# Kernel optimization log

Hardware: AMD Instinct MI355X
Metric: run time of the kernel (lower is better)

## Reference

```python
import jax, jax.numpy as jnp
import numpy as np
import math

B, S, DIN, DOUT, H, L, R, E = 8, 512, 256, 256, 8, 4, 8, 65536
N = B * S  # graph nodes = all tokens
DEPTH = DOUT // H


def setup_inputs() -> dict:
    key = jax.random.key(0)
    ks = jax.random.split(key, 16)
    s_in = 1.0 / math.sqrt(DIN)
    s_out = 1.0 / math.sqrt(DOUT)
    return {
        "x": jax.random.normal(ks[0], (B, S, DIN), jnp.float32),
        # graph structure (constant ints)
        "edge_src": jax.random.randint(ks[1], (E,), 0, N),
        "edge_dst": jax.random.randint(ks[2], (E,), 0, N),
        "edge_type": jax.random.randint(ks[3], (E,), 0, R),
        # linear: input_size -> output_size
        "Wl": jax.random.normal(ks[4], (DOUT, DIN), jnp.float32) * s_in,
        "bl": jnp.zeros((DOUT,), jnp.float32),
        # relational GAT params per layer / relation
        "Wgat": jax.random.normal(ks[5], (L, R, DOUT, DOUT), jnp.float32) * s_out,
        "a_src": jax.random.normal(ks[6], (L, R, DOUT), jnp.float32) * s_out,
        "a_dst": jax.random.normal(ks[7], (L, R, DOUT), jnp.float32) * s_out,
        # linear1: output_size -> input_size
        "W1": jax.random.normal(ks[8], (DIN, DOUT), jnp.float32) * s_out,
        "b1": jnp.zeros((DIN,), jnp.float32),
        # Wq, Wk: input_size -> output_size
        "Wq": jax.random.normal(ks[9], (DOUT, DIN), jnp.float32) * s_in,
        "bq": jnp.zeros((DOUT,), jnp.float32),
        "Wk": jax.random.normal(ks[10], (DOUT, DIN), jnp.float32) * s_in,
        "bk": jnp.zeros((DOUT,), jnp.float32),
    }


def _segment_softmax(e, dst, n):
    m = jax.ops.segment_max(e, dst, num_segments=n)
    ex = jnp.exp(e - m[dst])
    denom = jax.ops.segment_sum(ex, dst, num_segments=n)
    return ex / (denom[dst] + 1e-16)


def _rgat(h, Wgat, a_src, a_dst, edge_src, edge_dst, edge_type):
    # h: [N, DOUT]
    for l in range(L):
        # per-relation transform of all nodes: [R, N, D]
        hr = jnp.einsum('nd,rde->rne', h, Wgat[l])
        msg = hr[edge_type, edge_src]  # [E, D] gather by (relation, src)
        logits = (jnp.sum(a_src[l][edge_type] * msg, axis=-1)
                  + jnp.sum(a_dst[l][edge_type] * h[edge_dst], axis=-1))
        alpha = _segment_softmax(jax.nn.leaky_relu(logits, 0.2), edge_dst, N)
        agg = jax.ops.segment_sum(alpha[:, None] * msg, edge_dst, num_segments=N)
        h = jax.nn.elu(agg)
    return h


def reference(x, edge_src, edge_dst, edge_type, Wl, bl, Wgat, a_src, a_dst,
              W1, b1, Wq, bq, Wk, bk):
    h = x @ Wl.T + bl                       # [B, S, DOUT]
    h = h.reshape(N, DOUT)
    h = _rgat(h, Wgat, a_src, a_dst, edge_src, edge_dst, edge_type)
    h = h.reshape(B, S, DOUT)
    h = h @ W1.T + b1                       # [B, S, DIN]
    q = (h @ Wq.T + bq).reshape(B, S, H, DEPTH).transpose(0, 2, 1, 3)
    k = (h @ Wk.T + bk).reshape(B, S, H, DEPTH).transpose(0, 2, 1, 3)
    attn = jnp.einsum('bhqd,bhkd->bhqk', q, k) / math.sqrt(DEPTH)
    return attn
```

## Files before the change

kernel.cpp:

```cpp
#include <hip/hip_runtime.h>
#include <math.h>

#define NN 4096
#define D 256
#define RR 8
#define LL 4
#define EE 65536
#define BB 8
#define SS 512
#define HH 8

typedef short bf16x8 __attribute__((ext_vector_type(8)));
typedef float f32x4 __attribute__((ext_vector_type(4)));

__device__ __forceinline__ unsigned short f2bf(float f) {
  unsigned u = __float_as_uint(f);
  unsigned r = (u + 0x7fffu + ((u >> 16) & 1u)) >> 16;
  return (unsigned short)r;
}
__device__ __forceinline__ float bf2f(unsigned short s) {
  return __uint_as_float(((unsigned)s) << 16);
}

__device__ __forceinline__ void gload16(unsigned short* dst, const unsigned short* src) {
  __builtin_amdgcn_global_load_lds(
      (const __attribute__((address_space(1))) void*)src,
      (__attribute__((address_space(3))) void*)dst, 16, 0, 0);
}

template<int BM, int BN, bool F32OUT, bool SPLITOUT>
__global__ __launch_bounds__(256) void gemm_split(
    const unsigned short* __restrict__ Ah, const unsigned short* __restrict__ Al,
    const unsigned short* __restrict__ Bh, const unsigned short* __restrict__ Bl,
    const float* __restrict__ bias,
    float* __restrict__ C, unsigned short* __restrict__ Ch, unsigned short* __restrict__ Cl,
    int M, int N, int K)
{
  constexpr int MF = BM / 32;
  constexpr int NF = BN / 32;
  constexpr int ABUF = BM * 32;
  constexpr int BBUF = BN * 32;
  constexpr int BUFSZ = 2 * ABUF + 2 * BBUF;
  __shared__ unsigned short lds[2 * BUFSZ];

  const int t = threadIdx.x;
  const int lane = t & 63;
  const int w = t >> 6;
  const int wm = w >> 1, wn = w & 1;
  const int rb = blockIdx.y * BM;
  const int cb = blockIdx.x * BN;

  f32x4 acc[MF][NF];
#pragma unroll
  for (int m = 0; m < MF; ++m)
#pragma unroll
    for (int n = 0; n < NF; ++n)
      acc[m][n] = (f32x4){0.f, 0.f, 0.f, 0.f};

  const int srow = t >> 2;
  const int lslot = (t & 3) ^ ((srow >> 1) & 3);
  const unsigned short* gAh = Ah + (size_t)(rb + srow) * K + lslot * 8;
  const unsigned short* gAl = Al + (size_t)(rb + srow) * K + lslot * 8;
  const unsigned short* gBh = Bh + (size_t)(cb + srow) * K + lslot * 8;
  const unsigned short* gBl = Bl + (size_t)(cb + srow) * K + lslot * 8;

  auto stage = [&](int buf, int k0) {
    unsigned short* p = lds + buf * BUFSZ;
#pragma unroll
    for (int i = 0; i < BM / 64; ++i) {
      gload16(p + i * 2048 + t * 8,        gAh + (size_t)i * 64 * K + k0);
      gload16(p + ABUF + i * 2048 + t * 8, gAl + (size_t)i * 64 * K + k0);
    }
#pragma unroll
    for (int i = 0; i < BN / 64; ++i) {
      gload16(p + 2 * ABUF + i * 2048 + t * 8,        gBh + (size_t)i * 64 * K + k0);
      gload16(p + 2 * ABUF + BBUF + i * 2048 + t * 8, gBl + (size_t)i * 64 * K + k0);
    }
  };

  stage(0, 0);
  int cur = 0;
  for (int k0 = 0; k0 < K; k0 += 32) {
    __syncthreads();
    if (k0 + 32 < K) stage(cur ^ 1, k0 + 32);
    const unsigned short* p = lds + cur * BUFSZ;

    bf16x8 ah[MF], al[MF];
#pragma unroll
    for (int m = 0; m < MF; ++m) {
      int row = wm * (BM / 2) + m * 16 + (lane & 15);
      int off = row * 32 + (((lane >> 4) ^ ((row >> 1) & 3)) << 3);
      ah[m] = *(const bf16x8*)(p + off);
      al[m] = *(const bf16x8*)(p + ABUF + off);
    }
#pragma unroll
    for (int n = 0; n < NF; ++n) {
      int brow = wn * (BN / 2) + n * 16 + (lane & 15);
      int boff = brow * 32 + (((lane >> 4) ^ ((brow >> 1) & 3)) << 3);
      bf16x8 bh = *(const bf16x8*)(p + 2 * ABUF + boff);
      bf16x8 bl = *(const bf16x8*)(p + 2 * ABUF + BBUF + boff);
#pragma unroll
      for (int m = 0; m < MF; ++m) {
        acc[m][n] = __builtin_amdgcn_mfma_f32_16x16x32_bf16(ah[m], bh, acc[m][n], 0, 0, 0);
        acc[m][n] = __builtin_amdgcn_mfma_f32_16x16x32_bf16(al[m], bh, acc[m][n], 0, 0, 0);
        acc[m][n] = __builtin_amdgcn_mfma_f32_16x16x32_bf16(ah[m], bl, acc[m][n], 0, 0, 0);
      }
    }
    cur ^= 1;
  }

#pragma unroll
  for (int m = 0; m < MF; ++m) {
#pragma unroll
    for (int n = 0; n < NF; ++n) {
      int row0 = rb + wm * (BM / 2) + m * 16 + (lane >> 4) * 4;
      int col = cb + wn * (BN / 2) + n * 16 + (lane & 15);
      float bv = bias ? bias[col] : 0.f;
#pragma unroll
      for (int j = 0; j < 4; ++j) {
        float v = acc[m][n][j] + bv;
        size_t idx = (size_t)(row0 + j) * N + col;
        if (F32OUT) C[idx] = v;
        if (SPLITOUT) {
          unsigned short hb = f2bf(v);
          Ch[idx] = hb;
          Cl[idx] = f2bf(v - bf2f(hb));
        }
      }
    }
  }
}

__global__ __launch_bounds__(256) void cvt2_k(const float* __restrict__ x,
    unsigned short* __restrict__ xh, unsigned short* __restrict__ xl,
    const float* __restrict__ Wl,
    unsigned short* __restrict__ wlh, unsigned short* __restrict__ wll)
{
  const float* src; unsigned short* hi; unsigned short* lo; int i;
  if (blockIdx.x < 1024) { src = x;  hi = xh;  lo = xl;  i = blockIdx.x * 256 + threadIdx.x; }
  else                   { src = Wl; hi = wlh; lo = wll; i = (blockIdx.x - 1024) * 256 + threadIdx.x; }
  float4 v = ((const float4*)src)[i];
  ushort4 h, l;
  h.x = f2bf(v.x); l.x = f2bf(v.x - bf2f(h.x));
  h.y = f2bf(v.y); l.y = f2bf(v.y - bf2f(h.y));
  h.z = f2bf(v.z); l.z = f2bf(v.z - bf2f(h.z));
  h.w = f2bf(v.w); l.w = f2bf(v.w - bf2f(h.w));
  ((ushort4*)hi)[i] = h;
  ((ushort4*)lo)[i] = l;
}

__global__ __launch_bounds__(256) void transp_split_k(const float* __restrict__ W,
    unsigned short* __restrict__ th, unsigned short* __restrict__ tl)
{
  __shared__ float s[32][33];
  int g = blockIdx.z, bi = blockIdx.y, bj = blockIdx.x;
  int t = threadIdx.x;
  int r = t >> 3, c = (t & 7) * 4;
  float4 v = *(const float4*)(W + ((size_t)g * D + bi * 32 + r) * D + bj * 32 + c);
  s[r][c + 0] = v.x; s[r][c + 1] = v.y; s[r][c + 2] = v.z; s[r][c + 3] = v.w;
  __syncthreads();
  size_t ob = ((size_t)g * D + bj * 32 + r) * D + bi * 32 + c;
  ushort4 h, l;
  float o0 = s[c + 0][r], o1 = s[c + 1][r], o2 = s[c + 2][r], o3 = s[c + 3][r];
  h.x = f2bf(o0); l.x = f2bf(o0 - bf2f(h.x));
  h.y = f2bf(o1); l.y = f2bf(o1 - bf2f(h.y));
  h.z = f2bf(o2); l.z = f2bf(o2 - bf2f(h.z));
  h.w = f2bf(o3); l.w = f2bf(o3 - bf2f(h.w));
  *(ushort4*)(th + ob) = h;
  *(ushort4*)(tl + ob) = l;
}

__global__ void count_k(const int* __restrict__ ed, int* __restrict__ cnt) {
  int e = blockIdx.x * 256 + threadIdx.x;
  if (e < EE) atomicAdd(&cnt[ed[e]], 1);
}

__global__ __launch_bounds__(1024) void scan_k(const int* __restrict__ cnt,
    int* __restrict__ off, int* __restrict__ cur) {
  __shared__ int part[1024];
  int t = threadIdx.x;
  int base = t * 4;
  int c0 = cnt[base], c1 = cnt[base+1], c2 = cnt[base+2], c3 = cnt[base+3];
  int s = c0 + c1 + c2 + c3;
  part[t] = s;
  __syncthreads();
  for (int o = 1; o < 1024; o <<= 1) {
    int v = 0;
    if (t >= o) v = part[t - o];
    __syncthreads();
    part[t] += v;
    __syncthreads();
  }
  int excl = part[t] - s;
  off[base] = excl; off[base+1] = excl + c0; off[base+2] = excl + c0 + c1;
  off[base+3] = excl + c0 + c1 + c2;
  cur[base] = excl; cur[base+1] = excl + c0; cur[base+2] = excl + c0 + c1;
  cur[base+3] = excl + c0 + c1 + c2;
  if (t == 1023) off[NN] = EE;
}

__global__ void fill_k(const int* __restrict__ ed, int* __restrict__ cur,
                       int* __restrict__ csr) {
  int e = blockIdx.x * 256 + threadIdx.x;
  if (e < EE) { int p = atomicAdd(&cur[ed[e]], 1); csr[p] = e; }
}

__global__ __launch_bounds__(256) void wa_all_k(const float* __restrict__ Wg,
    const float* __restrict__ asrc, float* __restrict__ wa)
{
  int wid = blockIdx.x * 4 + (threadIdx.x >> 6);
  int lane = threadIdx.x & 63;
  int lr = wid >> 8, d = wid & 255;
  const float* row = Wg + ((size_t)lr * D + d) * D;
  const float* av = asrc + (size_t)lr * D;
  float s = 0.f;
  for (int i = lane; i < D; i += 64) s += row[i] * av[i];
#pragma unroll
  for (int o = 32; o; o >>= 1) s += __shfl_down(s, o);
  if (lane == 0) wa[wid] = s;
}

__global__ __launch_bounds__(256) void fold_k(const float* __restrict__ Wq,
    const float* __restrict__ Wk, const float* __restrict__ W1,
    unsigned short* __restrict__ fh, unsigned short* __restrict__ fl)
{
  int j = (blockIdx.x & 3) * 64 + (threadIdx.x & 63);
  int i = (blockIdx.x >> 2) * 4 + (threadIdx.x >> 6);
  const float* row = i < 256 ? Wq + (size_t)i * D : Wk + (size_t)(i - 256) * D;
  float s = 0.f;
  for (int k = 0; k < D; ++k) s += row[k] * W1[(size_t)k * D + j];
  size_t idx = (size_t)i * D + j;
  unsigned short hb = f2bf(s);
  fh[idx] = hb;
  fl[idx] = f2bf(s - bf2f(hb));
}

__global__ __launch_bounds__(256) void foldb_k(const float* __restrict__ Wq,
    const float* __restrict__ Wk, const float* __restrict__ b1,
    const float* __restrict__ bq, const float* __restrict__ bk,
    float* __restrict__ bqk)
{
  int idx = blockIdx.x * 4 + (threadIdx.x >> 6);
  int lane = threadIdx.x & 63;
  const float* row = idx < 256 ? Wq + (size_t)idx * D : Wk + (size_t)(idx - 256) * D;
  float s = 0.f;
  for (int i = lane; i < D; i += 64) s += row[i] * b1[i];
#pragma unroll
  for (int o = 32; o; o >>= 1) s += __shfl_down(s, o);
  if (lane == 0) bqk[idx] = s + (idx < 256 ? bq[idx] : bk[idx - 256]);
}

__global__ __launch_bounds__(256) void scores_split_k(
    const unsigned short* __restrict__ hh, const unsigned short* __restrict__ hl,
    const float* __restrict__ wa_l, const float* __restrict__ adst_l,
    float* __restrict__ ssrc, float* __restrict__ sdst)
{
  __shared__ float sh[256];
  int n = blockIdx.x, tid = threadIdx.x;
  size_t idx = (size_t)n * D + tid;
  sh[tid] = bf2f(hh[idx]) + bf2f(hl[idx]);
  __syncthreads();
  int wv = tid >> 6, lane = tid & 63;
#pragma unroll
  for (int rr = 0; rr < 2; ++rr) {
    int r = wv * 2 + rr;
    const float* wr = wa_l + (size_t)r * D;
    const float* ar = adst_l + (size_t)r * D;
    float s1 = sh[lane] * wr[lane] + sh[lane+64] * wr[lane+64]
             + sh[lane+128] * wr[lane+128] + sh[lane+192] * wr[lane+192];
    float s2 = sh[lane] * ar[lane] + sh[lane+64] * ar[lane+64]
             + sh[lane+128] * ar[lane+128] + sh[lane+192] * ar[lane+192];
#pragma unroll
    for (int o = 32; o; o >>= 1) { s1 += __shfl_down(s1, o); s2 += __shfl_down(s2, o); }
    if (lane == 0) { ssrc[(size_t)r * NN + n] = s1; sdst[(size_t)r * NN + n] = s2; }
  }
}

__global__ __launch_bounds__(256) void agg_fused_k(
    const int* __restrict__ csr, const int* __restrict__ off,
    const int* __restrict__ et, const int* __restrict__ es,
    const float* __restrict__ ssrc, const float* __restrict__ sdst,
    const float* __restrict__ hr2,
    unsigned short* __restrict__ hh, unsigned short* __restrict__ hl,
    const float* __restrict__ wa_next, const float* __restrict__ adst_next,
    float* __restrict__ ssrc_o, float* __restrict__ sdst_o)
{
  __shared__ float slog[1024];
  __shared__ int soff[1024];
  __shared__ float sdn[RR];
  __shared__ float red[8];
  __shared__ float wred[4][256];
  int n = blockIdx.x, tid = threadIdx.x;
  int o0 = off[n];
  int deg = off[n + 1] - o0;
  if (deg > 1024) deg = 1024;
  if (tid < RR) sdn[tid] = sdst[(size_t)tid * NN + n];
  __syncthreads();
  for (int i = tid; i < deg; i += 256) {
    int e = csr[o0 + i];
    int t = et[e], s = es[e];
    float v = ssrc[(size_t)t * NN + s] + sdn[t];
    slog[i] = v > 0.f ? v : 0.2f * v;
    soff[i] = s * (RR * D) + t * D;
  }
  __syncthreads();
  int lane = tid & 63, wv = tid >> 6;
  float lm = -INFINITY;
  for (int i = tid; i < deg; i += 256) lm = fmaxf(lm, slog[i]);
#pragma unroll
  for (int o = 32; o; o >>= 1) lm = fmaxf(lm, __shfl_xor(lm, o));
  if (lane == 0) red[wv] = lm;
  __syncthreads();
  float m = fmaxf(fmaxf(red[0], red[1]), fmaxf(red[2], red[3]));
  float ls = 0.f;
  for (int i = tid; i < deg; i += 256) {
    float a = expf(slog[i] - m);
    slog[i] = a;
    ls += a;
  }
#pragma unroll
  for (int o = 32; o; o >>= 1) ls += __shfl_xor(ls, o);
  if (lane == 0) red[4 + wv] = ls;
  __syncthreads();
  float dinv = 1.f / (red[4] + red[5] + red[6] + red[7] + 1e-16f);
  float a0 = 0.f, a1 = 0.f, a2 = 0.f, a3 = 0.f;
  for (int i = wv; i < deg; i += 4) {
    float al = slog[i];
    const float* row = hr2 + (size_t)soff[i];
    a0 += al * row[lane];
    a1 += al * row[lane + 64];
    a2 += al * row[lane + 128];
    a3 += al * row[lane + 192];
  }
  wred[wv][lane]       = a0;
  wred[wv][lane + 64]  = a1;
  wred[wv][lane + 128] = a2;
  wred[wv][lane + 192] = a3;
  __syncthreads();
  float acc = (wred[0][tid] + wred[1][tid]) + (wred[2][tid] + wred[3][tid]);
  acc *= dinv;
  float v = acc > 0.f ? acc : expm1f(acc);
  size_t idx = (size_t)n * D + tid;
  unsigned short hb = f2bf(v);
  hh[idx] = hb;
  hl[idx] = f2bf(v - bf2f(hb));

  if (wa_next) {
    __syncthreads();
    slog[tid] = v;
    __syncthreads();
#pragma unroll
    for (int rr2 = 0; rr2 < 2; ++rr2) {
      int r = wv * 2 + rr2;
      const float* wr = wa_next + (size_t)r * D;
      const float* ar = adst_next + (size_t)r * D;
      float s1 = slog[lane] * wr[lane] + slog[lane+64] * wr[lane+64]
               + slog[lane+128] * wr[lane+128] + slog[lane+192] * wr[lane+192];
      float s2 = slog[lane] * ar[lane] + slog[lane+64] * ar[lane+64]
               + slog[lane+128] * ar[lane+128] + slog[lane+192] * ar[lane+192];
#pragma unroll
      for (int o = 32; o; o >>= 1) { s1 += __shfl_down(s1, o); s2 += __shfl_down(s2, o); }
      if (lane == 0) { ssrc_o[(size_t)r * NN + n] = s1; sdst_o[(size_t)r * NN + n] = s2; }
    }
  }
}

__global__ __launch_bounds__(256) void attn_mfma_k(
    const unsigned short* __restrict__ qkh, const unsigned short* __restrict__ qkl,
    float* __restrict__ out)
{
  int bh = blockIdx.y; int b = bh >> 3, hd = bh & 7;
  int rb = (blockIdx.x >> 3) * 64, cb = (blockIdx.x & 7) * 64;
  int t = threadIdx.x, lane = t & 63, w = t >> 6;
  int wm = w >> 1, wn = w & 1;
  int colq = hd * 32 + (lane >> 4) * 8;
  int colk = 256 + colq;
  int arow = b * SS + rb + wm * 32 + (lane & 15);
  int brow = b * SS + cb + wn * 32 + (lane & 15);

  bf16x8 aH[2], aL[2], bH[2], bL[2];
#pragma unroll
  for (int m = 0; m < 2; ++m) {
    size_t o1 = (size_t)(arow + m * 16) * 512 + colq;
    aH[m] = *(const bf16x8*)(qkh + o1);
    aL[m] = *(const bf16x8*)(qkl + o1);
    size_t o2 = (size_t)(brow + m * 16) * 512 + colk;
    bH[m] = *(const bf16x8*)(qkh + o2);
    bL[m] = *(const bf16x8*)(qkl + o2);
  }
  f32x4 acc[2][2];
#pragma unroll
  for (int m = 0; m < 2; ++m)
#pragma unroll
    for (int n = 0; n < 2; ++n) {
      acc[m][n] = (f32x4){0.f, 0.f, 0.f, 0.f};
      acc[m][n] = __builtin_amdgcn_mfma_f32_16x16x32_bf16(aH[m], bH[n], acc[m][n], 0, 0, 0);
      acc[m][n] = __builtin_amdgcn_mfma_f32_16x16x32_bf16(aL[m], bH[n], acc[m][n], 0, 0, 0);
      acc[m][n] = __builtin_amdgcn_mfma_f32_16x16x32_bf16(aH[m], bL[n], acc[m][n], 0, 0, 0);
    }
  const float scale = 0.17677669529663687f;
  size_t ob = (size_t)bh * SS * SS;
#pragma unroll
  for (int m = 0; m < 2; ++m)
#pragma unroll
    for (int n = 0; n < 2; ++n) {
      int row0 = rb + wm * 32 + m * 16 + (lane >> 4) * 4;
      int col = cb + wn * 32 + n * 16 + (lane & 15);
#pragma unroll
      for (int j = 0; j < 4; ++j)
        out[ob + (size_t)(row0 + j) * SS + col] = acc[m][n][j] * scale;
    }
}

extern "C" void kernel_launch(void* const* d_in, const int* in_sizes, int n_in,
                              void* d_out, int out_size, void* d_ws, size_t ws_size,
                              hipStream_t stream) {
  const float* x    = (const float*)d_in[0];
  const int*   es   = (const int*)d_in[1];
  const int*   ed   = (const int*)d_in[2];
  const int*   et   = (const int*)d_in[3];
  const float* Wl   = (const float*)d_in[4];
  const float* bl   = (const float*)d_in[5];
  const float* Wgat = (const float*)d_in[6];
  const float* asr  = (const float*)d_in[7];
  const float* adt  = (const float*)d_in[8];
  const float* W1   = (const float*)d_in[9];
  const float* b1   = (const float*)d_in[10];
  const float* Wq   = (const float*)d_in[11];
  const float* bq   = (const float*)d_in[12];
  const float* Wk   = (const float*)d_in[13];
  const float* bk   = (const float*)d_in[14];
  float* out = (float*)d_out;

  char* w = (char*)d_ws;
  size_t o = 0;
  auto alloc = [&](size_t bytes) { void* p = w + o; o += (bytes + 255) & ~(size_t)255; return p; };
  unsigned short* hh    = (unsigned short*)alloc((size_t)NN * D * 2);
  unsigned short* hl    = (unsigned short*)alloc((size_t)NN * D * 2);
  unsigned short* Wgt_h = (unsigned short*)alloc((size_t)LL * RR * D * D * 2);
  unsigned short* Wgt_l = (unsigned short*)alloc((size_t)LL * RR * D * D * 2);
  unsigned short* wlh   = (unsigned short*)alloc((size_t)D * D * 2);
  unsigned short* wll   = (unsigned short*)alloc((size_t)D * D * 2);
  unsigned short* fqkh  = (unsigned short*)alloc((size_t)2 * D * D * 2);
  unsigned short* fqkl  = (unsigned short*)alloc((size_t)2 * D * D * 2);
  float* bqk   = (float*)alloc((size_t)2 * D * 4);
  float* wa    = (float*)alloc((size_t)LL * RR * D * 4);
  float* ssrcA = (float*)alloc((size_t)RR * NN * 4);
  float* sdstA = (float*)alloc((size_t)RR * NN * 4);
  float* ssrcB = (float*)alloc((size_t)RR * NN * 4);
  float* sdstB = (float*)alloc((size_t)RR * NN * 4);
  int*   cnt   = (int*)alloc((size_t)NN * 4);
  int*   off   = (int*)alloc((size_t)(NN + 1) * 4);
  int*   cur   = (int*)alloc((size_t)NN * 4);
  int*   csr   = (int*)alloc((size_t)EE * 4);
  char* big = (char*)alloc((size_t)NN * RR * D * 4);
  float*          hr2 = (float*)big;
  unsigned short* xh  = (unsigned short*)big;
  unsigned short* xl  = (unsigned short*)(big + (size_t)NN * D * 2);
  unsigned short* qkh = (unsigned short*)big;
  unsigned short* qkl = (unsigned short*)(big + (size_t)NN * 512 * 2);

  hipMemsetAsync(cnt, 0, NN * sizeof(int), stream);
  count_k<<<EE / 256, 256, 0, stream>>>(ed, cnt);
  scan_k<<<1, 1024, 0, stream>>>(cnt, off, cur);
  fill_k<<<EE / 256, 256, 0, stream>>>(ed, cur, csr);

  cvt2_k<<<1024 + 64, 256, 0, stream>>>(x, xh, xl, Wl, wlh, wll);
  transp_split_k<<<dim3(8, 8, LL * RR), 256, 0, stream>>>(Wgat, Wgt_h, Wgt_l);
  wa_all_k<<<LL * RR * D / 4, 256, 0, stream>>>(Wgat, asr, wa);
  fold_k<<<512, 256, 0, stream>>>(Wq, Wk, W1, fqkh, fqkl);
  foldb_k<<<128, 256, 0, stream>>>(Wq, Wk, b1, bq, bk, bqk);

  gemm_split<64, 64, false, true><<<dim3(4, 64), 256, 0, stream>>>(
      xh, xl, wlh, wll, bl, nullptr, hh, hl, NN, D, D);
  scores_split_k<<<NN, 256, 0, stream>>>(hh, hl, wa, adt, ssrcA, sdstA);

  for (int l = 0; l < LL; ++l) {
    gemm_split<128, 128, true, false><<<dim3(16, 32), 256, 0, stream>>>(
        hh, hl, Wgt_h + (size_t)l * RR * D * D, Wgt_l + (size_t)l * RR * D * D,
        nullptr, hr2, nullptr, nullptr, NN, RR * D, D);
    const float* wan = (l < LL - 1) ? wa + (size_t)(l + 1) * RR * D : nullptr;
    const float* adn = (l < LL - 1) ? adt + (size_t)(l + 1) * RR * D : nullptr;
    const float* sin_ = (l & 1) ? ssrcB : ssrcA;
    const float* din_ = (l & 1) ? sdstB : sdstA;
    float* sou_ = (l & 1) ? ssrcA : ssrcB;
    float* dou_ = (l & 1) ? sdstA : sdstB;
    agg_fused_k<<<NN, 256, 0, stream>>>(csr, off, et, es, sin_, din_, hr2,
                                        hh, hl, wan, adn, sou_, dou_);
  }

  gemm_split<64, 64, false, true><<<dim3(8, 64), 256, 0, stream>>>(
      hh, hl, fqkh, fqkl, bqk, nullptr, qkh, qkl, NN, 512, D);

  attn_mfma_k<<<dim3(64, BB * HH), 256, 0, stream>>>(qkh, qkl, out);
}
```

Before: 242.5 us.

## Add specialized RGAT GEMM, merge prep kernels, vectorize aggregation loads

Replaces the generic split-bf16 GEMM for the per-layer relation transform with a dedicated 128-thread kernel. It uses a double-buffered LDS pipeline, swizzled layout and larger per-wave tiles. The five separate weight-prep kernels are merged into one launch, and the wa projection is now computed with atomics inside the transpose blocks, so wa is zeroed in count_k. The aggregation inner loop now uses float4 row loads. This cuts launch overhead and aims for better GEMM efficiency, at the cost of lower occupancy (launch_bounds 128,1) and atomic float accumulation order.

```diff
diff --git a/kernel.cpp b/kernel.cpp
--- a/kernel.cpp
+++ b/kernel.cpp
@@ -9,6 +9,8 @@
 #define BB 8
 #define SS 512
 #define HH 8
+#define RK 256
+#define RN 2048
 
 typedef short bf16x8 __attribute__((ext_vector_type(8)));
 typedef float f32x4 __attribute__((ext_vector_type(4)));
@@ -131,46 +133,93 @@
   }
 }
 
-__global__ __launch_bounds__(256) void cvt2_k(const float* __restrict__ x,
-    unsigned short* __restrict__ xh, unsigned short* __restrict__ xl,
-    const float* __restrict__ Wl,
-    unsigned short* __restrict__ wlh, unsigned short* __restrict__ wll)
+__global__ __launch_bounds__(128, 1) void gemm_rgat(
+    const unsigned short* __restrict__ Ah, const unsigned short* __restrict__ Al,
+    const unsigned short* __restrict__ Bh, const unsigned short* __restrict__ Bl,
+    float* __restrict__ C)
 {
-  const float* src; unsigned short* hi; unsigned short* lo; int i;
-  if (blockIdx.x < 1024) { src = x;  hi = xh;  lo = xl;  i = blockIdx.x * 256 + threadIdx.x; }
-  else                   { src = Wl; hi = wlh; lo = wll; i = (blockIdx.x - 1024) * 256 + threadIdx.x; }
-  float4 v = ((const float4*)src)[i];
-  ushort4 h, l;
-  h.x = f2bf(v.x); l.x = f2bf(v.x - bf2f(h.x));
-  h.y = f2bf(v.y); l.y = f2bf(v.y - bf2f(h.y));
-  h.z = f2bf(v.z); l.z = f2bf(v.z - bf2f(h.z));
-  h.w = f2bf(v.w); l.w = f2bf(v.w - bf2f(h.w));
-  ((ushort4*)hi)[i] = h;
-  ((ushort4*)lo)[i] = l;
-}
-
-__global__ __launch_bounds__(256) void transp_split_k(const float* __restrict__ W,
-    unsigned short* __restrict__ th, unsigned short* __restrict__ tl)
-{
-  __shared__ float s[32][33];
-  int g = blockIdx.z, bi = blockIdx.y, bj = blockIdx.x;
-  int t = threadIdx.x;
-  int r = t >> 3, c = (t & 7) * 4;
-  float4 v = *(const float4*)(W + ((size_t)g * D + bi * 32 + r) * D + bj * 32 + c);
-  s[r][c + 0] = v.x; s[r][c + 1] = v.y; s[r][c + 2] = v.z; s[r][c + 3] = v.w;
-  __syncthreads();
-  size_t ob = ((size_t)g * D + bj * 32 + r) * D + bi * 32 + c;
-  ushort4 h, l;
-  float o0 = s[c + 0][r], o1 = s[c + 1][r], o2 = s[c + 2][r], o3 = s[c + 3][r];
-  h.x = f2bf(o0); l.x = f2bf(o0 - bf2f(h.x));
-  h.y = f2bf(o1); l.y = f2bf(o1 - bf2f(h.y));
-  h.z = f2bf(o2); l.z = f2bf(o2 - bf2f(h.z));
-  h.w = f2bf(o3); l.w = f2bf(o3 - bf2f(h.w));
-  *(ushort4*)(th + ob) = h;
-  *(ushort4*)(tl + ob) = l;
-}
-
-__global__ void count_k(const int* __restrict__ ed, int* __restrict__ cnt) {
+  constexpr int ABUF = 128 * 32;
+  constexpr int BUFSZ = 4 * ABUF;
+  __shared__ unsigned short lds[2 * BUFSZ];
+
+  const int t = threadIdx.x;
+  const int lane = t & 63;
+  const int wm = t >> 6;
+  const int rb = blockIdx.y * 128;
+  const int cb = blockIdx.x * 128;
+
+  f32x4 acc[4][8];
+#pragma unroll
+  for (int m = 0; m < 4; ++m)
+#pragma unroll
+    for (int n = 0; n < 8; ++n)
+      acc[m][n] = (f32x4){0.f, 0.f, 0.f, 0.f};
+
+  const int srow = t >> 2;
+  const int lslot = (t & 3) ^ ((srow >> 1) & 3);
+  const unsigned short* gAh = Ah + (size_t)(rb + srow) * RK + lslot * 8;
+  const unsigned short* gAl = Al + (size_t)(rb + srow) * RK + lslot * 8;
+  const unsigned short* gBh = Bh + (size_t)(cb + srow) * RK + lslot * 8;
+  const unsigned short* gBl = Bl + (size_t)(cb + srow) * RK + lslot * 8;
+
+  auto stage = [&](int buf, int k0) {
+    unsigned short* p = lds + buf * BUFSZ;
+#pragma unroll
+    for (int i = 0; i < 4; ++i) {
+      gload16(p + i * 1024 + t * 8,            gAh + (size_t)i * 32 * RK + k0);
+      gload16(p + ABUF + i * 1024 + t * 8,     gAl + (size_t)i * 32 * RK + k0);
+      gload16(p + 2 * ABUF + i * 1024 + t * 8, gBh + (size_t)i * 32 * RK + k0);
+      gload16(p + 3 * ABUF + i * 1024 + t * 8, gBl + (size_t)i * 32 * RK + k0);
+    }
+  };
+
+  stage(0, 0);
+  int cur = 0;
+  for (int k0 = 0; k0 < RK; k0 += 32) {
+    __syncthreads();
+    if (k0 + 32 < RK) stage(cur ^ 1, k0 + 32);
+    const unsigned short* p = lds + cur * BUFSZ;
+
+    bf16x8 ah[4], al[4];
+#pragma unroll
+    for (int m = 0; m < 4; ++m) {
+      int row = wm * 64 + m * 16 + (lane & 15);
+      int off = row * 32 + (((lane >> 4) ^ ((row >> 1) & 3)) << 3);
+      ah[m] = *(const bf16x8*)(p + off);
+      al[m] = *(const bf16x8*)(p + ABUF + off);
+    }
+#pragma unroll
+    for (int n = 0; n < 8; ++n) {
+      int brow = n * 16 + (lane & 15);
+      int boff = brow * 32 + (((lane >> 4) ^ ((brow >> 1) & 3)) << 3);
+      bf16x8 bh = *(const bf16x8*)(p + 2 * ABUF + boff);
+      bf16x8 bl = *(const bf16x8*)(p + 3 * ABUF + boff);
+#pragma unroll
+      for (int m = 0; m < 4; ++m) {
+        acc[m][n] = __builtin_amdgcn_mfma_f32_16x16x32_bf16(ah[m], bh, acc[m][n], 0, 0, 0);
+        acc[m][n] = __builtin_amdgcn_mfma_f32_16x16x32_bf16(al[m], bh, acc[m][n], 0, 0, 0);
+        acc[m][n] = __builtin_amdgcn_mfma_f32_16x16x32_bf16(ah[m], bl, acc[m][n], 0, 0, 0);
+      }
+    }
+    cur ^= 1;
+  }
+
+#pragma unroll
+  for (int m = 0; m < 4; ++m) {
+#pragma unroll
+    for (int n = 0; n < 8; ++n) {
+      int row0 = rb + wm * 64 + m * 16 + (lane >> 4) * 4;
+      int col = cb + n * 16 + (lane & 15);
+#pragma unroll
+      for (int j = 0; j < 4; ++j)
+        C[(size_t)(row0 + j) * RN + col] = acc[m][n][j];
+    }
+  }
+}
+
+__global__ void count_k(const int* __restrict__ ed, int* __restrict__ cnt,
+                        float* __restrict__ wa) {
+  if (blockIdx.x < 32) wa[blockIdx.x * 256 + threadIdx.x] = 0.f;
   int e = blockIdx.x * 256 + threadIdx.x;
   if (e < EE) atomicAdd(&cnt[ed[e]], 1);
 }
@@ -205,49 +254,76 @@
   if (e < EE) { int p = atomicAdd(&cur[ed[e]], 1); csr[p] = e; }
 }
 
-__global__ __launch_bounds__(256) void wa_all_k(const float* __restrict__ Wg,
-    const float* __restrict__ asrc, float* __restrict__ wa)
+__global__ __launch_bounds__(256) void prep_k(
+    const float* __restrict__ x, unsigned short* __restrict__ xh, unsigned short* __restrict__ xl,
+    const float* __restrict__ Wl, unsigned short* __restrict__ wlh, unsigned short* __restrict__ wll,
+    const float* __restrict__ Wq, const float* __restrict__ Wk, const float* __restrict__ W1,
+    unsigned short* __restrict__ fqkh, unsigned short* __restrict__ fqkl,
+    const float* __restrict__ b1, const float* __restrict__ bq, const float* __restrict__ bk,
+    float* __restrict__ bqk,
+    const float* __restrict__ Wgat, const float* __restrict__ asrc,
+    unsigned short* __restrict__ th, unsigned short* __restrict__ tl,
+    float* __restrict__ wa)
 {
-  int wid = blockIdx.x * 4 + (threadIdx.x >> 6);
-  int lane = threadIdx.x & 63;
-  int lr = wid >> 8, d = wid & 255;
-  const float* row = Wg + ((size_t)lr * D + d) * D;
-  const float* av = asrc + (size_t)lr * D;
-  float s = 0.f;
-  for (int i = lane; i < D; i += 64) s += row[i] * av[i];
-#pragma unroll
-  for (int o = 32; o; o >>= 1) s += __shfl_down(s, o);
-  if (lane == 0) wa[wid] = s;
-}
-
-__global__ __launch_bounds__(256) void fold_k(const float* __restrict__ Wq,
-    const float* __restrict__ Wk, const float* __restrict__ W1,
-    unsigned short* __restrict__ fh, unsigned short* __restrict__ fl)
-{
-  int j = (blockIdx.x & 3) * 64 + (threadIdx.x & 63);
-  int i = (blockIdx.x >> 2) * 4 + (threadIdx.x >> 6);
-  const float* row = i < 256 ? Wq + (size_t)i * D : Wk + (size_t)(i - 256) * D;
-  float s = 0.f;
-  for (int k = 0; k < D; ++k) s += row[k] * W1[(size_t)k * D + j];
-  size_t idx = (size_t)i * D + j;
-  unsigned short hb = f2bf(s);
-  fh[idx] = hb;
-  fl[idx] = f2bf(s - bf2f(hb));
-}
-
-__global__ __launch_bounds__(256) void foldb_k(const float* __restrict__ Wq,
-    const float* __restrict__ Wk, const float* __restrict__ b1,
-    const float* __restrict__ bq, const float* __restrict__ bk,
-    float* __restrict__ bqk)
-{
-  int idx = blockIdx.x * 4 + (threadIdx.x >> 6);
-  int lane = threadIdx.x & 63;
-  const float* row = idx < 256 ? Wq + (size_t)idx * D : Wk + (size_t)(idx - 256) * D;
-  float s = 0.f;
-  for (int i = lane; i < D; i += 64) s += row[i] * b1[i];
-#pragma unroll
-  for (int o = 32; o; o >>= 1) s += __shfl_down(s, o);
-  if (lane == 0) bqk[idx] = s + (idx < 256 ? bq[idx] : bk[idx - 256]);
+  __shared__ float s[32][33];
+  int b = blockIdx.x, t = threadIdx.x;
+  if (b < 1088) {
+    const float* src; unsigned short* hi; unsigned short* lo; int i;
+    if (b < 1024) { src = x;  hi = xh;  lo = xl;  i = b * 256 + t; }
+    else          { src = Wl; hi = wlh; lo = wll; i = (b - 1024) * 256 + t; }
+    float4 v = ((const float4*)src)[i];
+    ushort4 h, l;
+    h.x = f2bf(v.x); l.x = f2bf(v.x - bf2f(h.x));
+    h.y = f2bf(v.y); l.y = f2bf(v.y - bf2f(h.y));
+    h.z = f2bf(v.z); l.z = f2bf(v.z - bf2f(h.z));
+    h.w = f2bf(v.w); l.w = f2bf(v.w - bf2f(h.w));
+    ((ushort4*)hi)[i] = h;
+    ((ushort4*)lo)[i] = l;
+  } else if (b < 1600) {
+    int b2 = b - 1088;
+    int j = (b2 & 3) * 64 + (t & 63);
+    int i = (b2 >> 2) * 4 + (t >> 6);
+    const float* row = i < 256 ? Wq + (size_t)i * D : Wk + (size_t)(i - 256) * D;
+    float sm = 0.f;
+    for (int k = 0; k < D; ++k) sm += row[k] * W1[(size_t)k * D + j];
+    size_t idx = (size_t)i * D + j;
+    unsigned short hb = f2bf(sm);
+    fqkh[idx] = hb;
+    fqkl[idx] = f2bf(sm - bf2f(hb));
+  } else if (b < 1728) {
+    int b2 = b - 1600;
+    int idx = b2 * 4 + (t >> 6);
+    int lane = t & 63;
+    const float* row = idx < 256 ? Wq + (size_t)idx * D : Wk + (size_t)(idx - 256) * D;
+    float sm = 0.f;
+    for (int i = lane; i < D; i += 64) sm += row[i] * b1[i];
+#pragma unroll
+    for (int o = 32; o; o >>= 1) sm += __shfl_down(sm, o);
+    if (lane == 0) bqk[idx] = sm + (idx < 256 ? bq[idx] : bk[idx - 256]);
+  } else {
+    int b2 = b - 1728;
+    int g = b2 >> 6, bi = (b2 >> 3) & 7, bj = b2 & 7;
+    int r = t >> 3, c = (t & 7) * 4;
+    float4 v = *(const float4*)(Wgat + ((size_t)g * D + bi * 32 + r) * D + bj * 32 + c);
+    s[r][c + 0] = v.x; s[r][c + 1] = v.y; s[r][c + 2] = v.z; s[r][c + 3] = v.w;
+    __syncthreads();
+    size_t ob = ((size_t)g * D + bj * 32 + r) * D + bi * 32 + c;
+    ushort4 h, l4;
+    float o0 = s[c + 0][r], o1 = s[c + 1][r], o2 = s[c + 2][r], o3 = s[c + 3][r];
+    h.x = f2bf(o0); l4.x = f2bf(o0 - bf2f(h.x));
+    h.y = f2bf(o1); l4.y = f2bf(o1 - bf2f(h.y));
+    h.z = f2bf(o2); l4.z = f2bf(o2 - bf2f(h.z));
+    h.w = f2bf(o3); l4.w = f2bf(o3 - bf2f(h.w));
+    *(ushort4*)(th + ob) = h;
+    *(ushort4*)(tl + ob) = l4;
+    if (t < 32) {
+      const float* av = asrc + (size_t)g * D + bj * 32;
+      float p2 = 0.f;
+#pragma unroll
+      for (int cc = 0; cc < 32; ++cc) p2 += s[t][cc] * av[cc];
+      atomicAdd(&wa[(size_t)g * D + bi * 32 + t], p2);
+    }
+  }
 }
 
 __global__ __launch_bounds__(256) void scores_split_k(
@@ -323,19 +399,13 @@
   if (lane == 0) red[4 + wv] = ls;
   __syncthreads();
   float dinv = 1.f / (red[4] + red[5] + red[6] + red[7] + 1e-16f);
-  float a0 = 0.f, a1 = 0.f, a2 = 0.f, a3 = 0.f;
+  float4 a4 = make_float4(0.f, 0.f, 0.f, 0.f);
   for (int i = wv; i < deg; i += 4) {
     float al = slog[i];
-    const float* row = hr2 + (size_t)soff[i];
-    a0 += al * row[lane];
-    a1 += al * row[lane + 64];
-    a2 += al * row[lane + 128];
-    a3 += al * row[lane + 192];
-  }
-  wred[wv][lane]       = a0;
-  wred[wv][lane + 64]  = a1;
-  wred[wv][lane + 128] = a2;
-  wred[wv][lane + 192] = a3;
+    float4 rv = ((const float4*)(hr2 + (size_t)soff[i]))[lane];
+    a4.x += al * rv.x; a4.y += al * rv.y; a4.z += al * rv.z; a4.w += al * rv.w;
+  }
+  ((float4*)wred[wv])[lane] = a4;
   __syncthreads();
   float acc = (wred[0][tid] + wred[1][tid]) + (wred[2][tid] + wred[3][tid]);
   acc *= dinv;
@@ -461,24 +531,21 @@
   unsigned short* qkl = (unsigned short*)(big + (size_t)NN * 512 * 2);
 
   hipMemsetAsync(cnt, 0, NN * sizeof(int), stream);
-  count_k<<<EE / 256, 256, 0, stream>>>(ed, cnt);
+  count_k<<<EE / 256, 256, 0, stream>>>(ed, cnt, wa);
   scan_k<<<1, 1024, 0, stream>>>(cnt, off, cur);
   fill_k<<<EE / 256, 256, 0, stream>>>(ed, cur, csr);
 
-  cvt2_k<<<1024 + 64, 256, 0, stream>>>(x, xh, xl, Wl, wlh, wll);
-  transp_split_k<<<dim3(8, 8, LL * RR), 256, 0, stream>>>(Wgat, Wgt_h, Wgt_l);
-  wa_all_k<<<LL * RR * D / 4, 256, 0, stream>>>(Wgat, asr, wa);
-  fold_k<<<512, 256, 0, stream>>>(Wq, Wk, W1, fqkh, fqkl);
-  foldb_k<<<128, 256, 0, stream>>>(Wq, Wk, b1, bq, bk, bqk);
+  prep_k<<<3776, 256, 0, stream>>>(x, xh, xl, Wl, wlh, wll, Wq, Wk, W1,
+                                   fqkh, fqkl, b1, bq, bk, bqk,
+                                   Wgat, asr, Wgt_h, Wgt_l, wa);
 
   gemm_split<64, 64, false, true><<<dim3(4, 64), 256, 0, stream>>>(
       xh, xl, wlh, wll, bl, nullptr, hh, hl, NN, D, D);
   scores_split_k<<<NN, 256, 0, stream>>>(hh, hl, wa, adt, ssrcA, sdstA);
 
   for (int l = 0; l < LL; ++l) {
-    gemm_split<128, 128, true, false><<<dim3(16, 32), 256, 0, stream>>>(
-        hh, hl, Wgt_h + (size_t)l * RR * D * D, Wgt_l + (size_t)l * RR * D * D,
-        nullptr, hr2, nullptr, nullptr, NN, RR * D, D);
+    gemm_rgat<<<dim3(RN / 128, NN / 128), 128, 0, stream>>>(
+        hh, hl, Wgt_h + (size_t)l * RR * D * D, Wgt_l + (size_t)l * RR * D * D, hr2);
     const float* wan = (l < LL - 1) ? wa + (size_t)(l + 1) * RR * D : nullptr;
     const float* adn = (l < LL - 1) ? adt + (size_t)(l + 1) * RR * D : nullptr;
     const float* sin_ = (l & 1) ? ssrcB : ssrcA;
```

Measured after the change: 226.3 us. -6.7%, faster.
